# Performance work log

Measured on AMD Instinct MI355X. Metric: run time of the kernel, lower is better.

The kernel has to match this reference:

```python
import jax, jax.numpy as jnp
import numpy as np

N = 50000        # nodes
N_EDGES = 800000 # edges before self loops
D_IN = 128       # in_features
D_OUT = 64       # out_features (per head)
H = 2            # heads
NEG_SLOPE = 0.2  # GATv2Conv default negative_slope
EPS = 1e-5       # LayerNorm eps


def setup_inputs() -> dict:
    key = jax.random.key(0)
    ks = jax.random.split(key, 8)
    X = jax.random.normal(ks[0], (N, D_IN), jnp.float32)
    E = jax.random.randint(ks[1], (2, N_EDGES), 0, N, dtype=jnp.int32)
    attr = jax.random.normal(ks[2], (N_EDGES,), jnp.float32)
    # GATv2Conv params: lin_l / lin_r (share_weights=False, bias=True), att, concat bias
    s_in = 1.0 / np.sqrt(D_IN)
    W_l = jax.random.normal(ks[3], (D_IN, H * D_OUT), jnp.float32) * s_in
    b_l = jnp.zeros((H * D_OUT,), jnp.float32)
    W_r = jax.random.normal(ks[4], (D_IN, H * D_OUT), jnp.float32) * s_in
    b_r = jnp.zeros((H * D_OUT,), jnp.float32)
    att = jax.random.normal(ks[5], (H, D_OUT), jnp.float32) * (1.0 / np.sqrt(D_OUT))
    bias = jnp.zeros((H * D_OUT,), jnp.float32)
    # final_linear + LayerNorm params
    W_f = jax.random.normal(ks[6], (H * D_OUT, D_OUT), jnp.float32) * (1.0 / np.sqrt(H * D_OUT))
    b_f = jnp.zeros((D_OUT,), jnp.float32)
    gamma = jnp.ones((D_OUT,), jnp.float32)
    beta = jnp.zeros((D_OUT,), jnp.float32)
    return dict(X=X, E=E, attr=attr, W_l=W_l, b_l=b_l, W_r=W_r, b_r=b_r,
                att=att, bias=bias, W_f=W_f, b_f=b_f, gamma=gamma, beta=beta)


def _forward(X, E, W_l, b_l, W_r, b_r, att, bias, W_f, b_f, gamma, beta):
    # add self loops (PyG GATv2Conv default add_self_loops=True)
    loop = jnp.arange(N, dtype=E.dtype)
    src = jnp.concatenate([E[0], loop])  # [Et]
    dst = jnp.concatenate([E[1], loop])  # [Et]
    x_l = (X @ W_l + b_l).reshape(N, H, D_OUT)  # source-side transform
    x_r = (X @ W_r + b_r).reshape(N, H, D_OUT)  # target-side transform
    # per-edge GATv2 score: a^T LeakyReLU(x_i + x_j)
    s = jax.nn.leaky_relu(x_l[src] + x_r[dst], NEG_SLOPE)      # [Et, H, C]
    alpha = jnp.einsum('ehc,hc->eh', s, att)                   # [Et, H]
    # segment softmax over incoming edges of each target node
    a_max = jax.ops.segment_max(alpha, dst, num_segments=N)    # [N, H]
    a_max = jnp.where(jnp.isfinite(a_max), a_max, 0.0)
    num = jnp.exp(alpha - a_max[dst])
    den = jax.ops.segment_sum(num, dst, num_segments=N)
    w = num / den[dst]                                         # [Et, H]
    # weighted scatter-aggregate of source messages
    out = jax.ops.segment_sum(x_l[src] * w[:, :, None], dst, num_segments=N)  # [N,H,C]
    out = out.reshape(N, H * D_OUT) + bias                     # concat heads + bias
    # final linear + LayerNorm
    h = out @ W_f + b_f                                        # [N, D_OUT]
    mu = jnp.mean(h, axis=-1, keepdims=True)
    var = jnp.mean((h - mu) ** 2, axis=-1, keepdims=True)
    return (h - mu) * jax.lax.rsqrt(var + EPS) * gamma + beta


def reference(X, E, attr, W_l, b_l, W_r, b_r, att, bias, W_f, b_f, gamma, beta):
    H_out = _forward(X, E, W_l, b_l, W_r, b_r, att, bias, W_f, b_f, gamma, beta)
    return (H_out, E, attr)
```

## Files before the change

kernel.cpp:

```cpp
#include <hip/hip_runtime.h>

typedef unsigned short u16;
typedef unsigned int   u32;


#define DIN   128
#define DOUT  64
#define HD    128
#define BCAP  64

typedef __attribute__((ext_vector_type(8))) _Float16 f16x8;
typedef __attribute__((ext_vector_type(2))) _Float16 h2;
typedef __attribute__((ext_vector_type(4))) float    f32x4;

union H2U { u32 u; h2 h; };
__device__ __forceinline__ h2  U2H(u32 u) { H2U x; x.u = u; return x.h; }
__device__ __forceinline__ u32 H2Ub(h2 h) { H2U x; x.h = h; return x.u; }

__device__ __forceinline__ u16 f2h(float f) {
    _Float16 h = (_Float16)f;
    u16 r; __builtin_memcpy(&r, &h, 2); return r;
}

__device__ __forceinline__ u32 pkmax(u32 a, u32 b) {
    u32 d;
    asm("v_pk_max_f16 %0, %1, %2" : "=v"(d) : "v"(a), "v"(b));
    return d;
}

__device__ __forceinline__ float fdot2f(h2 a, h2 b, float c) {
#if __has_builtin(__builtin_amdgcn_fdot2)
    return __builtin_amdgcn_fdot2(a, b, c, false);
#else
    return c + (float)a[0] * (float)b[0] + (float)a[1] * (float)b[1];
#endif
}

__global__ void k_prep(const float* __restrict__ Wl, const float* __restrict__ Wr,
                       const float* __restrict__ Wf, const int* __restrict__ E,
                       const float* __restrict__ attr,
                       u16* __restrict__ WTl, u16* __restrict__ WTr,
                       uint4* __restrict__ Wfp, int* __restrict__ count,
                       float* __restrict__ out, int N, int NE)
{
    int i = blockIdx.x * 256 + threadIdx.x;
    if (i < N) { count[i] = 0; return; }
    int j = i - N;
    if (j < 16384) {
        int k = j >> 7, c = j & 127;
        WTl[c * 128 + k] = f2h(Wl[j]);
    } else if (j < 32768) {
        int t = j - 16384;
        int k = t >> 7, c = t & 127;
        WTr[c * 128 + k] = f2h(Wr[t]);
    } else if (j < 33792) {
        int t = j - 32768;
        int k4 = t >> 5, c = t & 31;
        const float* wrow = Wf + (size_t)(4 * k4) * DOUT;
        u32 a0 = (u32)f2h(wrow[c])              | ((u32)f2h(wrow[DOUT + c]) << 16);
        u32 a1 = (u32)f2h(wrow[2 * DOUT + c])   | ((u32)f2h(wrow[3 * DOUT + c]) << 16);
        u32 a2 = (u32)f2h(wrow[c + 32])         | ((u32)f2h(wrow[DOUT + c + 32]) << 16);
        u32 a3 = (u32)f2h(wrow[2 * DOUT + c + 32]) | ((u32)f2h(wrow[3 * DOUT + c + 32]) << 16);
        Wfp[t] = make_uint4(a0, a1, a2, a3);
    } else {
        int p = j - 33792;
        const size_t base = (size_t)N * DOUT;
        if (p < 2 * NE)      out[base + p] = (float)E[p];
        else if (p < 3 * NE) out[base + p] = attr[p - 2 * NE];
    }
}

__global__ void k_scatter_x(const int* __restrict__ E, int* __restrict__ count,
                            u16* __restrict__ bucket, int N, int NE)
{
    const int b   = blockIdx.x;
    const int seg = b & 7;
    const int lo  = (int)((long long)seg       * N >> 3);
    const int hi  = (int)((long long)(seg + 1) * N >> 3);
    const int stride = (gridDim.x >> 3) * 256;

    for (int e = (b >> 3) * 256 + threadIdx.x; e < NE; e += stride) {
        int dst = E[NE + e];
        if ((u32)dst >= (u32)N) dst = 0;
        if (dst < lo || dst >= hi) continue;
        int src = E[e];
        if ((u32)src >= (u32)N) src = 0;
        int rank = atomicAdd(&count[dst], 1);
        if (rank < BCAP) bucket[(size_t)dst * BCAP + rank] = (u16)src;
    }
}

__global__ __launch_bounds__(256) void gemm1(
    const float* __restrict__ X,
    const u16* __restrict__ WTl, const float* __restrict__ bl,
    const u16* __restrict__ WTr, const float* __restrict__ br,
    u16* __restrict__ xl_p, u16* __restrict__ xr_p, int N)
{
    __shared__ u16 sX[64 * 136];

    const int tid  = threadIdx.x;
    const int row0 = blockIdx.x * 64;

    for (int idx = tid; idx < 64 * 32; idx += 256) {
        int r  = idx >> 5;
        int k4 = (idx & 31) << 2;
        int gr = row0 + r;
        float4 v = make_float4(0.f, 0.f, 0.f, 0.f);
        if (gr < N) v = *(const float4*)(X + (size_t)gr * DIN + k4);
        u32 p0 = (u32)f2h(v.x) | ((u32)f2h(v.y) << 16);
        u32 p1 = (u32)f2h(v.z) | ((u32)f2h(v.w) << 16);
        *(uint2*)&sX[r * 136 + k4] = make_uint2(p0, p1);
    }
    __syncthreads();

    const int wv   = tid >> 6;
    const int lane = tid & 63;
    const int m    = lane & 15;
    const int quad = lane >> 4;

    f16x8 bx[4];
    #pragma unroll
    for (int kc = 0; kc < 4; kc++)
        bx[kc] = *(const f16x8*)&sX[(wv * 16 + m) * 136 + kc * 32 + quad * 8];

    const int gn = row0 + wv * 16 + m;

    #pragma unroll
    for (int cb = 0; cb < 2; cb++) {
        const u16*   WT  = cb ? WTr : WTl;
        const float* bia = cb ? br  : bl;
        f32x4 acc[8] = {};
        #pragma unroll
        for (int kc = 0; kc < 4; kc++) {
            #pragma unroll
            for (int t = 0; t < 8; t++) {
                f16x8 aw = *(const f16x8*)&WT[(t * 16 + m) * 128 + kc * 32 + quad * 8];
                acc[t] = __builtin_amdgcn_mfma_f32_16x16x32_f16(aw, bx[kc], acc[t], 0, 0, 0);
            }
        }
        if (gn < N) {
            u16* dst = cb ? xr_p : xl_p;
            #pragma unroll
            for (int t = 0; t < 8; t++) {
                const int c0 = t * 16 + quad * 4;
                float4 bv = *(const float4*)(bia + c0);
                u32 p0 = (u32)f2h(acc[t][0] + bv.x) | ((u32)f2h(acc[t][1] + bv.y) << 16);
                u32 p1 = (u32)f2h(acc[t][2] + bv.z) | ((u32)f2h(acc[t][3] + bv.w) << 16);
                *(uint2*)(dst + (size_t)gn * HD + c0) = make_uint2(p0, p1);
            }
        }
    }
}

template<int D>
__device__ __forceinline__ void edge_block(
    int myidx, int j, int sgbase, const char* xbase,
    const h2* xr2, const h2* at2, h2 c02,
    h2* acc2, float& lden)
{
    uint4 q[D];
    #pragma unroll
    for (int b = 0; b < D; b++) {
        u32 off = (u32)__shfl(myidx, sgbase + j + 2 * b) << 8;
        q[b] = *(const uint4*)(xbase + off);
    }
    float sh[D];
    #pragma unroll
    for (int b = 0; b < D; b++) {
        h2 v0 = U2H(q[b].x) + xr2[0];
        h2 v1 = U2H(q[b].y) + xr2[1];
        h2 v2 = U2H(q[b].z) + xr2[2];
        h2 v3 = U2H(q[b].w) + xr2[3];
        v0 = U2H(pkmax(H2Ub(v0), H2Ub(v0 * c02)));
        v1 = U2H(pkmax(H2Ub(v1), H2Ub(v1 * c02)));
        v2 = U2H(pkmax(H2Ub(v2), H2Ub(v2 * c02)));
        v3 = U2H(pkmax(H2Ub(v3), H2Ub(v3 * c02)));
        float s = fdot2f(v0, at2[0], 0.f);
        s = fdot2f(v1, at2[1], s);
        s = fdot2f(v2, at2[2], s);
        s = fdot2f(v3, at2[3], s);
        sh[b] = s;
    }
    #pragma unroll
    for (int m = 4; m; m >>= 1) {
        #pragma unroll
        for (int b = 0; b < D; b++) sh[b] += __shfl_xor(sh[b], m);
    }
    #pragma unroll
    for (int b = 0; b < D; b++) {
        float p = exp2f(sh[b]);
        lden += p;
        _Float16 ph = (_Float16)p;
        h2 p2 = {ph, ph};
        acc2[0] += p2 * U2H(q[b].x);
        acc2[1] += p2 * U2H(q[b].y);
        acc2[2] += p2 * U2H(q[b].z);
        acc2[3] += p2 * U2H(q[b].w);
    }
}

__global__ __launch_bounds__(256, 6) void k_edge(
    const u16* __restrict__ xl_p, const u16* __restrict__ xr_p,
    const float* __restrict__ att, const float* __restrict__ bias,
    const uint4* __restrict__ Wfp, const float* __restrict__ bf,
    const float* __restrict__ gamma, const float* __restrict__ beta,
    const int* __restrict__ count, const u16* __restrict__ bucket,
    float* __restrict__ out, int N)
{
    __shared__ uint4 sWp[1024];
    __shared__ u32   sAggU[8 * 64];

    const int tid = threadIdx.x;
    for (int idx = tid; idx < 1024; idx += 256) sWp[idx] = Wfp[idx];
    __syncthreads();

    const int l      = tid & 63;
    const int half   = tid >> 5;
    const int hl     = tid & 31;
    const int g16    = l & 15;
    const int ch0    = g16 * 8;
    const int sgsel  = (l >> 4) & 1;
    const int sgbase = (l & 32) + sgsel;
    const int n      = blockIdx.x * 8 + half;
    const bool active = (n < N);

    const h2 c02 = {(_Float16)0.2f, (_Float16)0.2f};
    h2 at2[4], xr2[4];
    {
        const float L2E = 1.44269504f;
        float4 a0 = *(const float4*)(att + ch0);
        float4 a1 = *(const float4*)(att + ch0 + 4);
        at2[0] = h2{(_Float16)(a0.x * L2E), (_Float16)(a0.y * L2E)};
        at2[1] = h2{(_Float16)(a0.z * L2E), (_Float16)(a0.w * L2E)};
        at2[2] = h2{(_Float16)(a1.x * L2E), (_Float16)(a1.y * L2E)};
        at2[3] = h2{(_Float16)(a1.z * L2E), (_Float16)(a1.w * L2E)};
        uint4 pr = make_uint4(0, 0, 0, 0);
        if (active) pr = *(const uint4*)(xr_p + (size_t)n * HD + ch0);
        xr2[0] = U2H(pr.x); xr2[1] = U2H(pr.y);
        xr2[2] = U2H(pr.z); xr2[3] = U2H(pr.w);
    }

    h2 acc2[4] = {};
    float lden = 0.f;

    int cnt_b = 0;
    if (active) {
        cnt_b = count[n];
        if (cnt_b < 0) cnt_b = 0;
        if (cnt_b > BCAP) cnt_b = BCAP;
    }
    const int cnt = active ? cnt_b + 1 : 0;
    const u16* mybkt = bucket + (size_t)(active ? n : 0) * BCAP;

    const char* xbase = (const char*)xl_p + ch0 * 2;

    int done = 0;
    while (done < cnt) {
        int chunk = cnt - done; if (chunk > 32) chunk = 32;
        int myidx = 0;
        if (hl < chunk) {
            int gj = done + hl;
            myidx = (gj < cnt_b) ? (int)mybkt[gj] : n;
        }
        int j = 0;
        for (; j + 16 <= chunk; j += 16)
            edge_block<8>(myidx, j, sgbase, xbase, xr2, at2, c02, acc2, lden);
        if (j + 8 <= chunk) {
            edge_block<4>(myidx, j, sgbase, xbase, xr2, at2, c02, acc2, lden);
            j += 8;
        }
        if (j + 4 <= chunk) {
            edge_block<2>(myidx, j, sgbase, xbase, xr2, at2, c02, acc2, lden);
            j += 4;
        }
        for (; j < chunk; j += 2) {
            u32 off = (u32)__shfl(myidx, sgbase + j) << 8;
            uint4 q = *(const uint4*)(xbase + off);
            h2 v0 = U2H(q.x) + xr2[0];
            h2 v1 = U2H(q.y) + xr2[1];
            h2 v2 = U2H(q.z) + xr2[2];
            h2 v3 = U2H(q.w) + xr2[3];
            v0 = U2H(pkmax(H2Ub(v0), H2Ub(v0 * c02)));
            v1 = U2H(pkmax(H2Ub(v1), H2Ub(v1 * c02)));
            v2 = U2H(pkmax(H2Ub(v2), H2Ub(v2 * c02)));
            v3 = U2H(pkmax(H2Ub(v3), H2Ub(v3 * c02)));
            float s = fdot2f(v0, at2[0], 0.f);
            s = fdot2f(v1, at2[1], s);
            s = fdot2f(v2, at2[2], s);
            s = fdot2f(v3, at2[3], s);
            #pragma unroll
            for (int m = 4; m; m >>= 1) s += __shfl_xor(s, m);
            float p = (j + sgsel < chunk) ? exp2f(s) : 0.f;
            lden += p;
            _Float16 ph = (_Float16)p;
            h2 p2 = {ph, ph};
            acc2[0] += p2 * U2H(q.x);
            acc2[1] += p2 * U2H(q.y);
            acc2[2] += p2 * U2H(q.z);
            acc2[3] += p2 * U2H(q.w);
        }
        done += chunk;
    }

    #pragma unroll
    for (int i = 0; i < 4; i++) {
        u32 o = (u32)__shfl_xor((int)H2Ub(acc2[i]), 16);
        acc2[i] = acc2[i] + U2H(o);
    }
    lden += __shfl_xor(lden, 16);

    float rl = 1.f / fmaxf(lden, 1e-30f);
    if (!(l & 16)) {
        float4 b0 = *(const float4*)(bias + ch0);
        float4 b1 = *(const float4*)(bias + ch0 + 4);
        uint4 w;
        w.x = (u32)f2h((float)acc2[0][0] * rl + b0.x) |
              ((u32)f2h((float)acc2[0][1] * rl + b0.y) << 16);
        w.y = (u32)f2h((float)acc2[1][0] * rl + b0.z) |
              ((u32)f2h((float)acc2[1][1] * rl + b0.w) << 16);
        w.z = (u32)f2h((float)acc2[2][0] * rl + b1.x) |
              ((u32)f2h((float)acc2[2][1] * rl + b1.y) << 16);
        w.w = (u32)f2h((float)acc2[3][0] * rl + b1.z) |
              ((u32)f2h((float)acc2[3][1] * rl + b1.w) << 16);
        *(uint4*)&sAggU[half * 64 + g16 * 4] = w;
    }
    asm volatile("s_waitcnt lgkmcnt(0)" ::: "memory");

    float h0 = bf[hl], h1 = bf[hl + 32];
    #pragma unroll 8
    for (int k4 = 0; k4 < 32; k4++) {
        uint4 wp = sWp[k4 * 32 + hl];
        uint2 ag = *(const uint2*)&sAggU[half * 64 + k4 * 2];
        h0 = fdot2f(U2H(ag.x), U2H(wp.x), h0);
        h0 = fdot2f(U2H(ag.y), U2H(wp.y), h0);
        h1 = fdot2f(U2H(ag.x), U2H(wp.z), h1);
        h1 = fdot2f(U2H(ag.y), U2H(wp.w), h1);
    }

    float s1r = h0 + h1, s2r = h0 * h0 + h1 * h1;
    #pragma unroll
    for (int m = 16; m; m >>= 1) { s1r += __shfl_xor(s1r, m); s2r += __shfl_xor(s2r, m); }
    float mu  = s1r * (1.f / 64.f);
    float var = s2r * (1.f / 64.f) - mu * mu;
    float rs  = rsqrtf(fmaxf(var, 0.f) + 1e-5f);
    if (active) {
        out[(size_t)n * DOUT + hl]      = (h0 - mu) * rs * gamma[hl]      + beta[hl];
        out[(size_t)n * DOUT + hl + 32] = (h1 - mu) * rs * gamma[hl + 32] + beta[hl + 32];
    }
}

extern "C" void kernel_launch(void* const* d_in, const int* in_sizes, int n_in,
                              void* d_out, int out_size, void* d_ws, size_t ws_size,
                              hipStream_t stream) {
    const float* X    = (const float*)d_in[0];
    const int*   E    = (const int*)d_in[1];
    const float* attr = (const float*)d_in[2];
    const float* Wl   = (const float*)d_in[3];
    const float* bl   = (const float*)d_in[4];
    const float* Wr   = (const float*)d_in[5];
    const float* br   = (const float*)d_in[6];
    const float* att  = (const float*)d_in[7];
    const float* bias = (const float*)d_in[8];
    const float* Wf   = (const float*)d_in[9];
    const float* bf   = (const float*)d_in[10];
    const float* gamma= (const float*)d_in[11];
    const float* beta = (const float*)d_in[12];
    float* out = (float*)d_out;

    const int N  = in_sizes[0] / DIN;
    const int NE = in_sizes[1] / 2;
    const int GB = (N + 63) / 64;

    char* ws = (char*)d_ws;
    int* count      = (int*)ws;               ws += (size_t)N * 4;
    u16* bucket     = (u16*)ws;               ws += (size_t)N * BCAP * 2;
    u16* xl_p       = (u16*)ws;               ws += (size_t)N * HD * 2;
    u16* xr_p       = (u16*)ws;               ws += (size_t)N * HD * 2;
    u16* WTl        = (u16*)ws;               ws += 128 * 128 * 2;
    u16* WTr        = (u16*)ws;               ws += 128 * 128 * 2;
    uint4* Wfp      = (uint4*)ws;             ws += 1024 * 16;

    const int prep_items = N + 33792 + 3 * NE;
    k_prep<<<(prep_items + 255) / 256, 256, 0, stream>>>(
        Wl, Wr, Wf, E, attr, WTl, WTr, Wfp, count, out, N, NE);

    k_scatter_x<<<2048, 256, 0, stream>>>(E, count, bucket, N, NE);

    gemm1<<<GB, 256, 0, stream>>>(X, WTl, bl, WTr, br, xl_p, xr_p, N);

    k_edge<<<(N + 7) / 8, 256, 0, stream>>>(
        xl_p, xr_p, att, bias, Wfp, bf, gamma, beta, count, bucket, out, N);
}
```

Baseline: 233.2 us.

## Pair scatter segments with XCC via hardware id and dynamic chunk queues

The edge bucketing kernel now reads the XCC id from a hardware register and starts on the node segment matching its own XCC, so the atomics on count and bucket stay within one XCC's L2 slice. Edge chunks are claimed from per-segment work queues, and the block then moves on to the other segments in turn. The copy of E and attr into the output, previously done in the prep kernel, is moved to the end of the scatter kernel. This adds queue atomics and two block barriers per chunk, makes each segment scan all edges through the queue, and assumes the getreg encoding is correct on this hardware.

```diff
diff --git a/kernel.cpp b/kernel.cpp
--- a/kernel.cpp
+++ b/kernel.cpp
@@ -8,6 +8,7 @@
 #define DOUT  64
 #define HD    128
 #define BCAP  64
+#define CH    4096
 
 typedef __attribute__((ext_vector_type(8))) _Float16 f16x8;
 typedef __attribute__((ext_vector_type(2))) _Float16 h2;
@@ -36,12 +37,19 @@
 #endif
 }
 
+__device__ __forceinline__ u32 my_xcc() {
+#if __has_builtin(__builtin_amdgcn_s_getreg)
+    return __builtin_amdgcn_s_getreg((7u << 11) | 20u) & 7u;
+#else
+    return 0u;
+#endif
+}
+
 __global__ void k_prep(const float* __restrict__ Wl, const float* __restrict__ Wr,
-                       const float* __restrict__ Wf, const int* __restrict__ E,
-                       const float* __restrict__ attr,
+                       const float* __restrict__ Wf,
                        u16* __restrict__ WTl, u16* __restrict__ WTr,
                        uint4* __restrict__ Wfp, int* __restrict__ count,
-                       float* __restrict__ out, int N, int NE)
+                       int* __restrict__ q, int N)
 {
     int i = blockIdx.x * 256 + threadIdx.x;
     if (i < N) { count[i] = 0; return; }
@@ -62,31 +70,52 @@
         u32 a2 = (u32)f2h(wrow[c + 32])         | ((u32)f2h(wrow[DOUT + c + 32]) << 16);
         u32 a3 = (u32)f2h(wrow[2 * DOUT + c + 32]) | ((u32)f2h(wrow[3 * DOUT + c + 32]) << 16);
         Wfp[t] = make_uint4(a0, a1, a2, a3);
-    } else {
-        int p = j - 33792;
-        const size_t base = (size_t)N * DOUT;
-        if (p < 2 * NE)      out[base + p] = (float)E[p];
-        else if (p < 3 * NE) out[base + p] = attr[p - 2 * NE];
-    }
-}
-
-__global__ void k_scatter_x(const int* __restrict__ E, int* __restrict__ count,
-                            u16* __restrict__ bucket, int N, int NE)
+    } else if (j < 33800) {
+        q[j - 33792] = 0;
+    }
+}
+
+__global__ __launch_bounds__(256) void k_scatter_xq(
+    const int* __restrict__ E, const float* __restrict__ attr,
+    int* __restrict__ count, u16* __restrict__ bucket, int* __restrict__ q,
+    float* __restrict__ out, int N, int NE)
 {
-    const int b   = blockIdx.x;
-    const int seg = b & 7;
-    const int lo  = (int)((long long)seg       * N >> 3);
-    const int hi  = (int)((long long)(seg + 1) * N >> 3);
-    const int stride = (gridDim.x >> 3) * 256;
-
-    for (int e = (b >> 3) * 256 + threadIdx.x; e < NE; e += stride) {
-        int dst = E[NE + e];
-        if ((u32)dst >= (u32)N) dst = 0;
-        if (dst < lo || dst >= hi) continue;
-        int src = E[e];
-        if ((u32)src >= (u32)N) src = 0;
-        int rank = atomicAdd(&count[dst], 1);
-        if (rank < BCAP) bucket[(size_t)dst * BCAP + rank] = (u16)src;
+    __shared__ int sc;
+    const int tid = threadIdx.x;
+    const int nch = (NE + CH - 1) / CH;
+    const u32 xcc = my_xcc();
+
+    for (int pass = 0; pass < 8; pass++) {
+        const int s  = (int)((xcc + pass) & 7u);
+        const int lo = (int)((long long)s       * N >> 3);
+        const int hi = (int)((long long)(s + 1) * N >> 3);
+        for (;;) {
+            if (tid == 0) sc = atomicAdd(&q[s], 1);
+            __syncthreads();
+            const int c = sc;
+            __syncthreads();
+            if (c >= nch) break;
+            const int e_end = min(NE, (c + 1) * CH);
+            for (int e = c * CH + tid; e < e_end; e += 256) {
+                int dst = E[NE + e];
+                if ((u32)dst >= (u32)N) dst = 0;
+                if (dst < lo || dst >= hi) continue;
+                int src = E[e];
+                if ((u32)src >= (u32)N) src = 0;
+                int rank = atomicAdd(&count[dst], 1);
+                if (rank < BCAP) bucket[(size_t)dst * BCAP + rank] = (u16)src;
+            }
+        }
+    }
+
+    const size_t base = (size_t)N * DOUT;
+    const long long P = 3LL * NE;
+    const int nB = gridDim.x;
+    int p0 = (int)(((long long)blockIdx.x) * P / nB);
+    int p1 = (int)(((long long)blockIdx.x + 1) * P / nB);
+    for (int p = p0 + tid; p < p1; p += 256) {
+        if (p < 2 * NE) out[base + p] = (float)E[p];
+        else            out[base + p] = attr[p - 2 * NE];
     }
 }
 
@@ -379,12 +408,13 @@
     u16* WTl        = (u16*)ws;               ws += 128 * 128 * 2;
     u16* WTr        = (u16*)ws;               ws += 128 * 128 * 2;
     uint4* Wfp      = (uint4*)ws;             ws += 1024 * 16;
-
-    const int prep_items = N + 33792 + 3 * NE;
+    int* q          = (int*)ws;               ws += 64;
+
+    const int prep_items = N + 33800;
     k_prep<<<(prep_items + 255) / 256, 256, 0, stream>>>(
-        Wl, Wr, Wf, E, attr, WTl, WTr, Wfp, count, out, N, NE);
-
-    k_scatter_x<<<2048, 256, 0, stream>>>(E, count, bucket, N, NE);
+        Wl, Wr, Wf, WTl, WTr, Wfp, count, q, N);
+
+    k_scatter_xq<<<2048, 256, 0, stream>>>(E, attr, count, bucket, q, out, N, NE);
 
     gemm1<<<GB, 256, 0, stream>>>(X, WTl, bl, WTr, br, xl_p, xr_p, N);
 
```

New measurement: 421.3 us. +80.6%, slower.
